# Kernel optimization log

Measured on AMD Instinct MI355X. Metric: run time of the kernel, lower is better.

The kernel has to match this reference:

```python
import jax, jax.numpy as jnp
import numpy as np

N_NODES = 50000
N_EDGES = 800000
IN_DIM = 64
HID = 128
OUT_DIM = 128
N_LAYERS = 3
LN_EPS = 1e-5


def setup_inputs() -> dict:
    key = jax.random.key(0)
    ks = jax.random.split(key, 12)
    x = jax.random.normal(ks[0], (N_NODES, IN_DIM), dtype=jnp.float32)
    edge_index = jax.random.randint(ks[1], (2, N_EDGES), 0, N_NODES, dtype=jnp.int32)
    # parameters
    W_in = jax.random.normal(ks[2], (IN_DIM, HID), dtype=jnp.float32) / np.sqrt(IN_DIM)
    b_in = jnp.zeros((HID,), dtype=jnp.float32)
    W_layers = jax.random.normal(ks[3], (N_LAYERS, HID, HID), dtype=jnp.float32) / np.sqrt(HID)
    b_layers = jnp.zeros((N_LAYERS, HID), dtype=jnp.float32)
    ln_g = jnp.ones((N_LAYERS, HID), dtype=jnp.float32)
    ln_b = jnp.zeros((N_LAYERS, HID), dtype=jnp.float32)
    W_out = jax.random.normal(ks[4], (HID, OUT_DIM), dtype=jnp.float32) / np.sqrt(HID)
    b_out = jnp.zeros((OUT_DIM,), dtype=jnp.float32)
    return {
        "x": x, "edge_index": edge_index, "num_nodes_actual": 48000,
        "W_in": W_in, "b_in": b_in,
        "W_layers": W_layers, "b_layers": b_layers,
        "ln_g": ln_g, "ln_b": ln_b,
        "W_out": W_out, "b_out": b_out,
    }


def _layer_norm(h, g, b):
    mu = jnp.mean(h, axis=-1, keepdims=True)
    var = jnp.mean(jnp.square(h - mu), axis=-1, keepdims=True)
    return (h - mu) * jax.lax.rsqrt(var + LN_EPS) * g + b


def reference(x, edge_index, num_nodes_actual, W_in, b_in, W_layers, b_layers, ln_g, ln_b, W_out, b_out):
    n = x.shape[0]
    src, dst = edge_index[0], edge_index[1]
    # degree-normalized scatter-add aggregation (same for all layers)
    degree = jax.ops.segment_sum(jnp.ones_like(src, dtype=x.dtype), dst, num_segments=n)
    inv_deg = 1.0 / jnp.clip(degree, 1.0)[:, None]  # [N,1]

    h = x @ W_in + b_in  # [N, HID]
    for i in range(N_LAYERS):
        residual = h
        agg = jax.ops.segment_sum(h[src], dst, num_segments=n) * inv_deg
        h = (h + agg) @ W_layers[i] + b_layers[i]
        h = _layer_norm(h, ln_g[i], ln_b[i])
        h = jax.nn.relu(h)
        h = h + residual
    h = h @ W_out + b_out  # [N, OUT_DIM]
    # mean over actual (non-padding) nodes, keepdim
    return jnp.mean(h[:num_nodes_actual], axis=0, keepdims=True)  # [1, OUT_DIM]
```

## Files before the change

kernel.cpp:

```cpp
#include <hip/hip_runtime.h>

#define HID 128
#define INP 64
#define LN_EPS 1e-5f
#define RT 64

typedef __attribute__((ext_vector_type(8))) short bf16x8;
typedef __attribute__((ext_vector_type(4))) float f32x4;

__device__ __forceinline__ unsigned f2bf(float f) {
    unsigned u = __float_as_uint(f);
    return (u + 0x7FFFu + ((u >> 16) & 1u)) >> 16;
}
__device__ __forceinline__ float bflo(unsigned v) { return __uint_as_float(v << 16); }
__device__ __forceinline__ float bfhi(unsigned v) { return __uint_as_float(v & 0xFFFF0000u); }

__global__ __launch_bounds__(256) void k_count(const int* __restrict__ dst, int nE, int* __restrict__ cnt,
                                               int nEdgeThreads,
                                               const float* __restrict__ W_in, const float* __restrict__ W_l,
                                               unsigned short* __restrict__ Wt_in, unsigned short* __restrict__ Wt_l) {
    int t = blockIdx.x * 256 + threadIdx.x;
    if (t < nEdgeThreads) {
        int base = t * 16;
        if (base + 16 <= nE) {
#pragma unroll
            for (int j = 0; j < 4; ++j) {
                int4 d = *reinterpret_cast<const int4*>(dst + base + j * 4);
                atomicAdd(&cnt[d.x], 1);
                atomicAdd(&cnt[d.y], 1);
                atomicAdd(&cnt[d.z], 1);
                atomicAdd(&cnt[d.w], 1);
            }
        } else {
            for (int e = base; e < nE; ++e) atomicAdd(&cnt[dst[e]], 1);
        }
        return;
    }
    int i = t - nEdgeThreads;
    if (i < 128 * 64) {
        int col = i >> 6, k = i & 63;
        Wt_in[i] = (unsigned short)f2bf(W_in[(size_t)k * HID + col]);
    } else if (i < 128 * 64 + 3 * 128 * 128) {
        int j = i - 128 * 64;
        int l = j >> 14, r = j & 16383;
        int col = r >> 7, k = r & 127;
        Wt_l[j] = (unsigned short)f2bf(W_l[(size_t)l * 16384 + (size_t)k * HID + col]);
    }
}

__global__ void k_scan1(const int* __restrict__ cnt, int n, int* __restrict__ rowp, int* __restrict__ bsum) {
    __shared__ int s[256];
    int i = blockIdx.x * 256 + threadIdx.x;
    int v = (i < n) ? cnt[i] : 0;
    s[threadIdx.x] = v;
    __syncthreads();
    for (int off = 1; off < 256; off <<= 1) {
        int t = (threadIdx.x >= off) ? s[threadIdx.x - off] : 0;
        __syncthreads();
        s[threadIdx.x] += t;
        __syncthreads();
    }
    if (i < n) rowp[i] = s[threadIdx.x] - v;
    if (threadIdx.x == 255) bsum[blockIdx.x] = s[255];
}

__global__ void k_scan2(int* __restrict__ bsum, int nb) {
    __shared__ int s[256];
    int v = (threadIdx.x < nb) ? bsum[threadIdx.x] : 0;
    s[threadIdx.x] = v;
    __syncthreads();
    for (int off = 1; off < 256; off <<= 1) {
        int t = (threadIdx.x >= off) ? s[threadIdx.x - off] : 0;
        __syncthreads();
        s[threadIdx.x] += t;
        __syncthreads();
    }
    if (threadIdx.x < nb) bsum[threadIdx.x] = s[threadIdx.x] - v;
}

__global__ void k_scan3(int* __restrict__ rowp, const int* __restrict__ bsum, const int* __restrict__ cnt,
                        int n, int nE, int* __restrict__ cursor, float* __restrict__ invd) {
    int i = blockIdx.x * 256 + threadIdx.x;
    if (i < n) {
        int rp = rowp[i] + bsum[blockIdx.x];
        rowp[i] = rp;
        cursor[i] = rp;
        int c = cnt[i];
        invd[i] = 1.0f / (float)(c > 1 ? c : 1);
    } else if (i == n) {
        rowp[n] = nE;
    }
}

__global__ __launch_bounds__(256) void k_fill(const int* __restrict__ src, const int* __restrict__ dst, int nE,
                                              int* __restrict__ cursor, int* __restrict__ csrc) {
    int t = blockIdx.x * 256 + threadIdx.x;
    int base = t * 16;
    if (base + 16 <= nE) {
        int4 d[4], s[4];
#pragma unroll
        for (int j = 0; j < 4; ++j) {
            d[j] = *reinterpret_cast<const int4*>(dst + base + j * 4);
            s[j] = *reinterpret_cast<const int4*>(src + base + j * 4);
        }
        int p[16];
#pragma unroll
        for (int j = 0; j < 4; ++j) {
            p[j * 4 + 0] = atomicAdd(&cursor[d[j].x], 1);
            p[j * 4 + 1] = atomicAdd(&cursor[d[j].y], 1);
            p[j * 4 + 2] = atomicAdd(&cursor[d[j].z], 1);
            p[j * 4 + 3] = atomicAdd(&cursor[d[j].w], 1);
        }
#pragma unroll
        for (int j = 0; j < 4; ++j) {
            csrc[p[j * 4 + 0]] = s[j].x;
            csrc[p[j * 4 + 1]] = s[j].y;
            csrc[p[j * 4 + 2]] = s[j].z;
            csrc[p[j * 4 + 3]] = s[j].w;
        }
    } else if (base < nE) {
        for (int e = base; e < nE; ++e) {
            int pp = atomicAdd(&cursor[dst[e]], 1);
            csrc[pp] = src[e];
        }
    }
}

__global__ __launch_bounds__(256) void k_inproj(const float* __restrict__ x,
                                                const unsigned short* __restrict__ Wt,
                                                const float* __restrict__ b,
                                                unsigned* __restrict__ hout, int n) {
    __shared__ unsigned short xs[RT * INP];
    const int tid = threadIdx.x;
    const int row0 = blockIdx.x * RT;

#pragma unroll
    for (int j = 0; j < 2; ++j) {
        int fid = tid + j * 256;
        int r = fid >> 3, c = fid & 7;
        int grow = row0 + r;
        unsigned o[4] = {0, 0, 0, 0};
        if (grow < n) {
            float4 v0 = *reinterpret_cast<const float4*>(x + (size_t)grow * INP + c * 8);
            float4 v1 = *reinterpret_cast<const float4*>(x + (size_t)grow * INP + c * 8 + 4);
            o[0] = f2bf(v0.x) | (f2bf(v0.y) << 16);
            o[1] = f2bf(v0.z) | (f2bf(v0.w) << 16);
            o[2] = f2bf(v1.x) | (f2bf(v1.y) << 16);
            o[3] = f2bf(v1.z) | (f2bf(v1.w) << 16);
        }
        int sw = c ^ (r & 7);
        *reinterpret_cast<uint4*>(xs + r * INP + sw * 8) = make_uint4(o[0], o[1], o[2], o[3]);
    }
    __syncthreads();

    const int l = tid & 63;
    const int w = tid >> 6;
    const int l15 = l & 15, lg = l >> 4;
    const int xrow = w * 16 + l15;

    f32x4 acc[8];
#pragma unroll
    for (int t = 0; t < 8; ++t) acc[t] = (f32x4){0.f, 0.f, 0.f, 0.f};

#pragma unroll
    for (int kc = 0; kc < 2; ++kc) {
        int bc = (kc * 4 + lg) ^ (xrow & 7);
        bf16x8 bfrag = *reinterpret_cast<const bf16x8*>(xs + xrow * INP + bc * 8);
        const unsigned short* wp = Wt + (size_t)l15 * INP + kc * 32 + lg * 8;
        bf16x8 af[8];
#pragma unroll
        for (int t = 0; t < 8; ++t) af[t] = *reinterpret_cast<const bf16x8*>(wp + (size_t)t * 16 * INP);
#pragma unroll
        for (int t = 0; t < 8; ++t)
            acc[t] = __builtin_amdgcn_mfma_f32_16x16x32_bf16(af[t], bfrag, acc[t], 0, 0, 0);
    }

    int grow = row0 + xrow;
    if (grow < n) {
#pragma unroll
        for (int t = 0; t < 8; ++t) {
            int c0 = t * 16 + lg * 4;
            f32x4 bb = *reinterpret_cast<const f32x4*>(b + c0);
            f32x4 o = acc[t] + bb;
            uint2 p;
            p.x = f2bf(o.x) | (f2bf(o.y) << 16);
            p.y = f2bf(o.z) | (f2bf(o.w) << 16);
            *reinterpret_cast<uint2*>(hout + (size_t)grow * 64 + t * 8 + lg * 2) = p;
        }
    }
}

__global__ __launch_bounds__(256) void k_agg(const unsigned* __restrict__ hb, const int* __restrict__ rowp,
                                             const int* __restrict__ csrc, const float* __restrict__ invd,
                                             unsigned* __restrict__ aggx, int n) {
    int node = blockIdx.x * 4 + (threadIdx.x >> 6);
    if (node >= n) return;
    int lane = threadIdx.x & 63;
    int e0 = rowp[node], e1 = rowp[node + 1];
    int deg = e1 - e0;
    unsigned self = hb[(size_t)node * 64 + lane];
    float inv = invd[node];
    float ax = 0.f, ay = 0.f;

    for (int base = 0; base < deg; base += 64) {
        int m = deg - base;
        if (m > 64) m = 64;
        int myidx = (base + lane < deg) ? csrc[e0 + base + lane] : 0;
        int j = 0;
        for (; j + 8 <= m; j += 8) {
            int s0 = __shfl(myidx, j + 0);
            int s1 = __shfl(myidx, j + 1);
            int s2 = __shfl(myidx, j + 2);
            int s3 = __shfl(myidx, j + 3);
            int s4 = __shfl(myidx, j + 4);
            int s5 = __shfl(myidx, j + 5);
            int s6 = __shfl(myidx, j + 6);
            int s7 = __shfl(myidx, j + 7);
            unsigned v0 = hb[(size_t)s0 * 64 + lane];
            unsigned v1 = hb[(size_t)s1 * 64 + lane];
            unsigned v2 = hb[(size_t)s2 * 64 + lane];
            unsigned v3 = hb[(size_t)s3 * 64 + lane];
            unsigned v4 = hb[(size_t)s4 * 64 + lane];
            unsigned v5 = hb[(size_t)s5 * 64 + lane];
            unsigned v6 = hb[(size_t)s6 * 64 + lane];
            unsigned v7 = hb[(size_t)s7 * 64 + lane];
            ax += ((bflo(v0) + bflo(v1)) + (bflo(v2) + bflo(v3))) +
                  ((bflo(v4) + bflo(v5)) + (bflo(v6) + bflo(v7)));
            ay += ((bfhi(v0) + bfhi(v1)) + (bfhi(v2) + bfhi(v3))) +
                  ((bfhi(v4) + bfhi(v5)) + (bfhi(v6) + bfhi(v7)));
        }
        for (; j < m; ++j) {
            int s0 = __shfl(myidx, j);
            unsigned v = hb[(size_t)s0 * 64 + lane];
            ax += bflo(v);
            ay += bfhi(v);
        }
    }

    float xlo = bflo(self) + ax * inv;
    float xhi = bfhi(self) + ay * inv;
    unsigned o = f2bf(xlo) | (f2bf(xhi) << 16);
    int c = lane >> 2;
    int sw = c ^ (node & 7);
    aggx[(size_t)node * 64 + sw * 4 + (lane & 3)] = o;
}

__global__ __launch_bounds__(256) void k_layer(const unsigned* __restrict__ hin,
                                               unsigned* __restrict__ hout,
                                               const unsigned* __restrict__ aggx,
                                               const unsigned short* __restrict__ Wt,
                                               const float* __restrict__ bias, const float* __restrict__ g,
                                               const float* __restrict__ lnb, int n) {
    const int tid = threadIdx.x;
    const int row0 = blockIdx.x * RT;
    const int lane = tid & 63;
    const int w = tid >> 6;
    const int l15 = lane & 15, lg = lane >> 4;
    const int xrow = w * 16 + l15;
    const int grow = row0 + xrow;

    const unsigned short* xg = reinterpret_cast<const unsigned short*>(aggx) + (size_t)grow * HID;

    f32x4 acc[8];
#pragma unroll
    for (int t = 0; t < 8; ++t) acc[t] = (f32x4){0.f, 0.f, 0.f, 0.f};

#pragma unroll
    for (int kc = 0; kc < 4; ++kc) {
        int bc = (kc * 4 + lg) ^ (xrow & 7);
        bf16x8 bfrag = *reinterpret_cast<const bf16x8*>(xg + bc * 8);
        const unsigned short* wp = Wt + (size_t)l15 * HID + kc * 32 + lg * 8;
        bf16x8 af[8];
#pragma unroll
        for (int t = 0; t < 8; ++t) af[t] = *reinterpret_cast<const bf16x8*>(wp + (size_t)t * 16 * HID);
#pragma unroll
        for (int t = 0; t < 8; ++t)
            acc[t] = __builtin_amdgcn_mfma_f32_16x16x32_bf16(af[t], bfrag, acc[t], 0, 0, 0);
    }

    float s = 0.f, q = 0.f;
#pragma unroll
    for (int t = 0; t < 8; ++t) {
        int c0 = t * 16 + lg * 4;
        f32x4 bb = *reinterpret_cast<const f32x4*>(bias + c0);
        acc[t] = acc[t] + bb;
        s += acc[t].x + acc[t].y + acc[t].z + acc[t].w;
        q += acc[t].x * acc[t].x + acc[t].y * acc[t].y + acc[t].z * acc[t].z + acc[t].w * acc[t].w;
    }
    s += __shfl_xor(s, 16, 64);
    s += __shfl_xor(s, 32, 64);
    q += __shfl_xor(q, 16, 64);
    q += __shfl_xor(q, 32, 64);
    float mu = s * (1.0f / HID);
    float var = q * (1.0f / HID) - mu * mu;
    float rs = rsqrtf(var + LN_EPS);

    if (grow < n) {
#pragma unroll
        for (int t = 0; t < 8; ++t) {
            int c0 = t * 16 + lg * 4;
            uint2 rv = *reinterpret_cast<const uint2*>(hin + (size_t)grow * 64 + t * 8 + lg * 2);
            f32x4 gv = *reinterpret_cast<const f32x4*>(g + c0);
            f32x4 lb = *reinterpret_cast<const f32x4*>(lnb + c0);
            float o0 = fmaxf((acc[t].x - mu) * rs * gv.x + lb.x, 0.f) + bflo(rv.x);
            float o1 = fmaxf((acc[t].y - mu) * rs * gv.y + lb.y, 0.f) + bfhi(rv.x);
            float o2 = fmaxf((acc[t].z - mu) * rs * gv.z + lb.z, 0.f) + bflo(rv.y);
            float o3 = fmaxf((acc[t].w - mu) * rs * gv.w + lb.w, 0.f) + bfhi(rv.y);
            uint2 p;
            p.x = f2bf(o0) | (f2bf(o1) << 16);
            p.y = f2bf(o2) | (f2bf(o3) << 16);
            *reinterpret_cast<uint2*>(hout + (size_t)grow * 64 + t * 8 + lg * 2) = p;
        }
    }
}

__global__ __launch_bounds__(256) void k_rowsum(const unsigned* __restrict__ hb, const int* __restrict__ n_act_p,
                                                float* __restrict__ accum, int n) {
    __shared__ float sred[256 * 2];
    int na = *n_act_p;
    int row0 = blockIdx.x * 256;
    int c = threadIdx.x & 63;
    int sub = threadIdx.x >> 6;
    int rend = row0 + 256;
    if (rend > na) rend = na;
    float sx = 0.f, sy = 0.f;
    for (int r = row0 + sub; r < rend; r += 4) {
        unsigned v = hb[(size_t)r * 64 + c];
        sx += bflo(v);
        sy += bfhi(v);
    }
    sred[threadIdx.x * 2] = sx;
    sred[threadIdx.x * 2 + 1] = sy;
    __syncthreads();
    if (threadIdx.x < 64) {
        float tx = sred[threadIdx.x * 2] + sred[(threadIdx.x + 64) * 2] +
                   sred[(threadIdx.x + 128) * 2] + sred[(threadIdx.x + 192) * 2];
        float ty = sred[threadIdx.x * 2 + 1] + sred[(threadIdx.x + 64) * 2 + 1] +
                   sred[(threadIdx.x + 128) * 2 + 1] + sred[(threadIdx.x + 192) * 2 + 1];
        if (row0 < na) {
            atomicAdd(&accum[2 * threadIdx.x], tx);
            atomicAdd(&accum[2 * threadIdx.x + 1], ty);
        }
    }
}

__global__ void k_out(const float* __restrict__ accum, const int* __restrict__ n_act_p,
                      const float* __restrict__ W_out, const float* __restrict__ b_out,
                      float* __restrict__ out) {
    __shared__ float m[HID];
    int c = threadIdx.x;
    float na = (float)(*n_act_p);
    m[c] = accum[c] / na;
    __syncthreads();
    float s = b_out[c];
    for (int k = 0; k < HID; ++k) s += m[k] * W_out[k * HID + c];
    out[c] = s;
}

extern "C" void kernel_launch(void* const* d_in, const int* in_sizes, int n_in,
                              void* d_out, int out_size, void* d_ws, size_t ws_size,
                              hipStream_t stream) {
    const int n  = in_sizes[0] / INP;
    const int nE = in_sizes[1] / 2;
    const float* x    = (const float*)d_in[0];
    const int*   ei   = (const int*)d_in[1];
    const int*   src  = ei;
    const int*   dst  = ei + nE;
    const int*   nact = (const int*)d_in[2];
    const float* W_in = (const float*)d_in[3];
    const float* b_in = (const float*)d_in[4];
    const float* W_l  = (const float*)d_in[5];
    const float* b_l  = (const float*)d_in[6];
    const float* lng  = (const float*)d_in[7];
    const float* lnb  = (const float*)d_in[8];
    const float* W_o  = (const float*)d_in[9];
    const float* b_o  = (const float*)d_in[10];

    char* ws = (char*)d_ws;
    size_t off = 0;
    auto alloc = [&](size_t bytes) {
        void* p = ws + off;
        off = (off + bytes + 255) & ~((size_t)255);
        return p;
    };
    unsigned* hbA  = (unsigned*)alloc((size_t)n * 64 * 4);
    unsigned* hbB  = (unsigned*)alloc((size_t)n * 64 * 4);
    unsigned* aggx = (unsigned*)alloc((size_t)(n + RT) * 64 * 4);
    int*   cnt  = (int*)alloc((size_t)n * 4);
    int*   rowp = (int*)alloc((size_t)(n + 1) * 4);
    int*   curs = (int*)alloc((size_t)n * 4);
    float* invd = (float*)alloc((size_t)n * 4);
    int*   csrc = (int*)alloc((size_t)nE * 4);
    int*   bsum = (int*)alloc(1024);
    float* accum = (float*)alloc(HID * 4);
    unsigned short* Wt_in = (unsigned short*)alloc(128 * 64 * 2);
    unsigned short* Wt_l  = (unsigned short*)alloc(3 * 128 * 128 * 2);

    hipMemsetAsync(cnt, 0, (size_t)n * 4, stream);
    hipMemsetAsync(accum, 0, HID * 4, stream);

    int nb = (n + 255) / 256;
    int nEdgeThreads = (nE + 15) / 16;
    int nPrep = 128 * 64 + 3 * 128 * 128;
    int cpgrid = (nEdgeThreads + nPrep + 255) / 256;
    k_count<<<cpgrid, 256, 0, stream>>>(dst, nE, cnt, nEdgeThreads, W_in, W_l, Wt_in, Wt_l);
    k_scan1<<<nb, 256, 0, stream>>>(cnt, n, rowp, bsum);
    k_scan2<<<1, 256, 0, stream>>>(bsum, nb);
    k_scan3<<<nb, 256, 0, stream>>>(rowp, bsum, cnt, n, nE, curs, invd);
    k_fill<<<(nEdgeThreads + 255) / 256, 256, 0, stream>>>(src, dst, nE, curs, csrc);

    int tgrid = (n + RT - 1) / RT;
    k_inproj<<<tgrid, 256, 0, stream>>>(x, Wt_in, b_in, hbA, n);

    const unsigned* hin = hbA;
    unsigned* hout = hbB;
    for (int l = 0; l < 3; ++l) {
        k_agg<<<(n + 3) / 4, 256, 0, stream>>>(hin, rowp, csrc, invd, aggx, n);
        k_layer<<<tgrid, 256, 0, stream>>>(hin, hout, aggx,
                                           Wt_l + (size_t)l * 128 * 128,
                                           b_l + l * HID, lng + l * HID, lnb + l * HID, n);
        const unsigned* t = hout;
        hout = (unsigned*)hin;
        hin = t;
    }
    k_rowsum<<<(n + 255) / 256, 256, 0, stream>>>(hin, nact, accum, n);
    k_out<<<1, HID, 0, stream>>>(accum, nact, W_o, b_o, (float*)d_out);
}
```

Baseline: 307.8 us.

## Replace direct CSR fill with two-pass bucketed scatter by destination block

```diff
diff --git a/kernel.cpp b/kernel.cpp
--- a/kernel.cpp
+++ b/kernel.cpp
@@ -4,6 +4,7 @@
 #define INP 64
 #define LN_EPS 1e-5f
 #define RT 64
+#define SCAP 1024
 
 typedef __attribute__((ext_vector_type(8))) short bf16x8;
 typedef __attribute__((ext_vector_type(4))) float f32x4;
@@ -92,36 +93,56 @@
     }
 }
 
-__global__ __launch_bounds__(256) void k_fill(const int* __restrict__ src, const int* __restrict__ dst, int nE,
-                                              int* __restrict__ cursor, int* __restrict__ csrc) {
+__global__ __launch_bounds__(256) void k_bucket(const int* __restrict__ src, const int* __restrict__ dst, int nE,
+                                                int* __restrict__ bcur, int2* __restrict__ bbuf,
+                                                int* __restrict__ cursor, int* __restrict__ csrc) {
     int t = blockIdx.x * 256 + threadIdx.x;
-    int base = t * 16;
-    if (base + 16 <= nE) {
-        int4 d[4], s[4];
-#pragma unroll
-        for (int j = 0; j < 4; ++j) {
-            d[j] = *reinterpret_cast<const int4*>(dst + base + j * 4);
-            s[j] = *reinterpret_cast<const int4*>(src + base + j * 4);
-        }
-        int p[16];
-#pragma unroll
-        for (int j = 0; j < 4; ++j) {
-            p[j * 4 + 0] = atomicAdd(&cursor[d[j].x], 1);
-            p[j * 4 + 1] = atomicAdd(&cursor[d[j].y], 1);
-            p[j * 4 + 2] = atomicAdd(&cursor[d[j].z], 1);
-            p[j * 4 + 3] = atomicAdd(&cursor[d[j].w], 1);
-        }
-#pragma unroll
-        for (int j = 0; j < 4; ++j) {
-            csrc[p[j * 4 + 0]] = s[j].x;
-            csrc[p[j * 4 + 1]] = s[j].y;
-            csrc[p[j * 4 + 2]] = s[j].z;
-            csrc[p[j * 4 + 3]] = s[j].w;
+    int base = t * 8;
+    int slice = blockIdx.x & 7;
+    if (base + 8 <= nE) {
+        int4 d0 = *reinterpret_cast<const int4*>(dst + base);
+        int4 d1 = *reinterpret_cast<const int4*>(dst + base + 4);
+        int4 s0 = *reinterpret_cast<const int4*>(src + base);
+        int4 s1 = *reinterpret_cast<const int4*>(src + base + 4);
+        int ds[8] = {d0.x, d0.y, d0.z, d0.w, d1.x, d1.y, d1.z, d1.w};
+        int ss[8] = {s0.x, s0.y, s0.z, s0.w, s1.x, s1.y, s1.z, s1.w};
+#pragma unroll
+        for (int j = 0; j < 8; ++j) {
+            int b = ds[j] >> 7;
+            int pos = atomicAdd(&bcur[b * 8 + slice], 1);
+            if (pos < SCAP) {
+                bbuf[((size_t)(b * 8 + slice)) * SCAP + pos] = make_int2(ss[j], ds[j]);
+            } else {
+                int p = atomicAdd(&cursor[ds[j]], 1);
+                csrc[p] = ss[j];
+            }
         }
     } else if (base < nE) {
         for (int e = base; e < nE; ++e) {
-            int pp = atomicAdd(&cursor[dst[e]], 1);
-            csrc[pp] = src[e];
+            int d = dst[e], s = src[e];
+            int b = d >> 7;
+            int pos = atomicAdd(&bcur[b * 8 + slice], 1);
+            if (pos < SCAP) {
+                bbuf[((size_t)(b * 8 + slice)) * SCAP + pos] = make_int2(s, d);
+            } else {
+                int p = atomicAdd(&cursor[d], 1);
+                csrc[p] = s;
+            }
+        }
+    }
+}
+
+__global__ __launch_bounds__(256) void k_fill2(const int* __restrict__ bcur, const int2* __restrict__ bbuf,
+                                               int* __restrict__ cursor, int* __restrict__ csrc) {
+    int b = blockIdx.x >> 1;
+    int s0 = (blockIdx.x & 1) * 4;
+    for (int slice = s0; slice < s0 + 4; ++slice) {
+        int cnt = bcur[b * 8 + slice];
+        if (cnt > SCAP) cnt = SCAP;
+        for (int e = threadIdx.x; e < cnt; e += 256) {
+            int2 sd = bbuf[((size_t)(b * 8 + slice)) * SCAP + e];
+            int p = atomicAdd(&cursor[sd.y], 1);
+            csrc[p] = sd.x;
         }
     }
 }
@@ -383,6 +404,7 @@
         off = (off + bytes + 255) & ~((size_t)255);
         return p;
     };
+    const int nBuck = (n + 127) >> 7;
     unsigned* hbA  = (unsigned*)alloc((size_t)n * 64 * 4);
     unsigned* hbB  = (unsigned*)alloc((size_t)n * 64 * 4);
     unsigned* aggx = (unsigned*)alloc((size_t)(n + RT) * 64 * 4);
@@ -395,9 +417,12 @@
     float* accum = (float*)alloc(HID * 4);
     unsigned short* Wt_in = (unsigned short*)alloc(128 * 64 * 2);
     unsigned short* Wt_l  = (unsigned short*)alloc(3 * 128 * 128 * 2);
+    int*  bcur = (int*)alloc((size_t)nBuck * 8 * 4);
+    int2* bbuf = (int2*)alloc((size_t)nBuck * 8 * SCAP * 8);
 
     hipMemsetAsync(cnt, 0, (size_t)n * 4, stream);
     hipMemsetAsync(accum, 0, HID * 4, stream);
+    hipMemsetAsync(bcur, 0, (size_t)nBuck * 8 * 4, stream);
 
     int nb = (n + 255) / 256;
     int nEdgeThreads = (nE + 15) / 16;
@@ -407,7 +432,8 @@
     k_scan1<<<nb, 256, 0, stream>>>(cnt, n, rowp, bsum);
     k_scan2<<<1, 256, 0, stream>>>(bsum, nb);
     k_scan3<<<nb, 256, 0, stream>>>(rowp, bsum, cnt, n, nE, curs, invd);
-    k_fill<<<(nEdgeThreads + 255) / 256, 256, 0, stream>>>(src, dst, nE, curs, csrc);
+    k_bucket<<<(nE / 8 + 255) / 256 + 1, 256, 0, stream>>>(src, dst, nE, bcur, bbuf, curs, csrc);
+    k_fill2<<<nBuck * 2, 256, 0, stream>>>(bcur, bbuf, curs, csrc);
 
     int tgrid = (n + RT - 1) / RT;
     k_inproj<<<tgrid, 256, 0, stream>>>(x, Wt_in, b_in, hbA, n);
```

After: 365.5 us. 1.19x slower.
